# Optimization experiments

Hardware: AMD Instinct MI355X
Metric: run time of the kernel (lower is better)

Reference implementation:

```python
import jax, jax.numpy as jnp
import numpy as np

D = 64      # hidden_dim
H = 4       # num_attention_heads
DH = D // H # head_dim
B = 64      # graphs per batch
SCALE = np.float32(np.sqrt(DH))


def _sage(x, edge, wl, bl, wr):
    # SAGEConv: lin_l(mean_j x_j) + lin_r(x_i); mean over incoming edges (dst = edge[1])
    src, dst = edge[0], edge[1]
    n = x.shape[0]
    agg = jax.ops.segment_sum(x[src], dst, num_segments=n)
    cnt = jax.ops.segment_sum(jnp.ones((edge.shape[1],), x.dtype), dst, num_segments=n)
    mean = agg / jnp.maximum(cnt, 1.0)[:, None]
    return mean @ wl + bl + x @ wr


def _cross_attn(xq, xk, w, b):
    # w: [3, D, D] stacked (Q, K, V) projections; b: [3, D]
    Q = (xq @ w[0] + b[0]).reshape(-1, H, DH)  # [Nq, H, DH]
    K = (xk @ w[1] + b[1]).reshape(-1, H, DH)  # [Nk, H, DH]
    V = (xk @ w[2] + b[2]).reshape(-1, H, DH)
    scores = jnp.einsum('qhd,khd->hqk', Q, K) / SCALE  # [H, Nq, Nk]
    wgt = jax.nn.softmax(scores, axis=-1)
    out = jnp.einsum('hqk,khd->qhd', wgt, V)
    return out.reshape(xq.shape[0], D)


def _segment_mean(x, seg, num):
    s = jax.ops.segment_sum(x, seg, num_segments=num)
    c = jax.ops.segment_sum(jnp.ones((x.shape[0],), x.dtype), seg, num_segments=num)
    return s / jnp.maximum(c, 1.0)[:, None]


def setup_inputs() -> dict:
    key = jax.random.key(0)
    ks = jax.random.split(key, 32)
    N_MOL, N_PROT, E_MOL, E_PROT = 2048, 8192, 32768, 131072
    MOL_IN, PROT_IN = 32, 64

    def lin(k, i, o, s=None):
        s = 1.0 / np.sqrt(i) if s is None else s
        return (jax.random.normal(k, (i, o), jnp.float32) * s)

    inp = {
        'x_mol': jax.random.normal(ks[0], (N_MOL, MOL_IN), jnp.float32),
        'x_prot': jax.random.normal(ks[1], (N_PROT, PROT_IN), jnp.float32),
        'm1_wl': lin(ks[2], MOL_IN, D), 'm1_bl': jnp.zeros((D,), jnp.float32), 'm1_wr': lin(ks[3], MOL_IN, D),
        'm2_wl': lin(ks[4], D, D), 'm2_bl': jnp.zeros((D,), jnp.float32), 'm2_wr': lin(ks[5], D, D),
        'p1_wl': lin(ks[6], PROT_IN, D), 'p1_bl': jnp.zeros((D,), jnp.float32), 'p1_wr': lin(ks[7], PROT_IN, D),
        'p2_wl': lin(ks[8], D, D), 'p2_bl': jnp.zeros((D,), jnp.float32), 'p2_wr': lin(ks[9], D, D),
        'amp_w': jax.random.normal(ks[10], (3, D, D), jnp.float32) / np.sqrt(D),
        'amp_b': jnp.zeros((3, D), jnp.float32),
        'apm_w': jax.random.normal(ks[11], (3, D, D), jnp.float32) / np.sqrt(D),
        'apm_b': jnp.zeros((3, D), jnp.float32),
        'fc1_w': lin(ks[12], 2 * D, D), 'fc1_b': jnp.zeros((D,), jnp.float32),
        'fc2_w': lin(ks[13], D, 1), 'fc2_b': jnp.zeros((1,), jnp.float32),
        'edge_mol': jax.random.randint(ks[14], (2, E_MOL), 0, N_MOL, jnp.int32),
        'edge_prot': jax.random.randint(ks[15], (2, E_PROT), 0, N_PROT, jnp.int32),
        'batch_mol': jnp.sort(jax.random.randint(ks[16], (N_MOL,), 0, B, jnp.int32)),
        'batch_prot': jnp.sort(jax.random.randint(ks[17], (N_PROT,), 0, B, jnp.int32)),
    }
    return inp


def reference(x_mol, x_prot,
              m1_wl, m1_bl, m1_wr, m2_wl, m2_bl, m2_wr,
              p1_wl, p1_bl, p1_wr, p2_wl, p2_bl, p2_wr,
              amp_w, amp_b, apm_w, apm_b,
              fc1_w, fc1_b, fc2_w, fc2_b,
              edge_mol, edge_prot, batch_mol, batch_prot):
    # two SAGE conv blocks per graph, ReLU after each (HeteroConv with one edge type)
    h_mol = jax.nn.relu(_sage(x_mol, edge_mol, m1_wl, m1_bl, m1_wr))
    h_mol = jax.nn.relu(_sage(h_mol, edge_mol, m2_wl, m2_bl, m2_wr))
    h_prot = jax.nn.relu(_sage(x_prot, edge_prot, p1_wl, p1_bl, p1_wr))
    h_prot = jax.nn.relu(_sage(h_prot, edge_prot, p2_wl, p2_bl, p2_wr))
    # cross attention (mol queries prot, prot queries mol) + residual
    h_mol_c = h_mol + _cross_attn(h_mol, h_prot, amp_w, amp_b)
    h_prot_c = h_prot + _cross_attn(h_prot, h_mol, apm_w, apm_b)
    # global mean pool per graph
    z_mol = _segment_mean(h_mol_c, batch_mol, B)    # [B, D]
    z_prot = _segment_mean(h_prot_c, batch_prot, B)  # [B, D]
    z = jnp.concatenate([z_mol, z_prot], axis=1)     # [B, 2D]
    x = jax.nn.relu(z @ fc1_w + fc1_b)
    out = jax.nn.sigmoid(x @ fc2_w + fc2_b)
    return out.squeeze(-1)  # [B]
```

## Files before the change

kernel.cpp:

```cpp
#include <hip/hip_runtime.h>
#include <math.h>

#define D 64
#define NB 64

typedef __attribute__((ext_vector_type(8))) short bf16x8;
typedef __attribute__((ext_vector_type(4))) float f32x4;
typedef __attribute__((ext_vector_type(16))) float f32x16;

#define M3(a, b, c) fmaxf(fmaxf((a), (b)), (c))

__device__ __forceinline__ unsigned short f2bf(float f) {
    unsigned u = __float_as_uint(f);
    u += 0x7FFF + ((u >> 16) & 1);
    return (unsigned short)(u >> 16);
}
__device__ __forceinline__ unsigned pk_bf16(float lo, float hi) {
    unsigned r;
    asm("v_cvt_pk_bf16_f32 %0, %1, %2" : "=v"(r) : "v"(lo), "v"(hi));
    return r;
}
__device__ __forceinline__ float fexp2(float x) {
    float r;
    asm("v_exp_f32 %0, %1" : "=v"(r) : "v"(x));
    return r;
}

__global__ void k_prep2(const int* __restrict__ em, int Em,
                        const int* __restrict__ ep, int Ep,
                        int* __restrict__ degm, int* __restrict__ degp,
                        const int* __restrict__ bm, int Nm, int* __restrict__ bsM,
                        const int* __restrict__ bp, int Np, int* __restrict__ bsP) {
    int i = blockIdx.x * blockDim.x + threadIdx.x;
    if (i < Em) atomicAdd(&degm[em[Em + i]], 1);
    int j = i - Em;
    if (j >= 0 && j < Ep) atomicAdd(&degp[ep[Ep + j]], 1);
    if (i < Nm) {
        int cur = bm[i];
        int prev = (i == 0) ? -1 : bm[i - 1];
        for (int b = prev + 1; b <= cur; ++b) bsM[b] = i;
        if (i == Nm - 1)
            for (int b = cur + 1; b <= NB; ++b) bsM[b] = Nm;
    }
    int j2 = i - Nm;
    if (j2 >= 0 && j2 < Np) {
        int cur = bp[j2];
        int prev = (j2 == 0) ? -1 : bp[j2 - 1];
        for (int b = prev + 1; b <= cur; ++b) bsP[b] = j2;
        if (j2 == Np - 1)
            for (int b = cur + 1; b <= NB; ++b) bsP[b] = Np;
    }
}

__global__ __launch_bounds__(256) void k_scan2(
        const int* __restrict__ degm, int Nm, int* __restrict__ rpm, int* __restrict__ curm,
        const int* __restrict__ degp, int Np, int* __restrict__ rpp, int* __restrict__ curp) {
    __shared__ int sdeg[8192];
    __shared__ int chunk[256];
    const int* deg = blockIdx.x ? degp : degm;
    int N = blockIdx.x ? Np : Nm;
    int* rowptr = blockIdx.x ? rpp : rpm;
    int* cursor = blockIdx.x ? curp : curm;
    int t = threadIdx.x;
    for (int i = t; i < N; i += 256) sdeg[i] = deg[i];
    __syncthreads();
    int C = (N + 255) / 256;
    int start = t * C;
    int sum = 0;
    for (int i = 0; i < C; ++i)
        if (start + i < N) sum += sdeg[start + i];
    chunk[t] = sum;
    __syncthreads();
    for (int ofs = 1; ofs < 256; ofs <<= 1) {
        int v = (t >= ofs) ? chunk[t - ofs] : 0;
        __syncthreads();
        chunk[t] += v;
        __syncthreads();
    }
    int base = (t == 0) ? 0 : chunk[t - 1];
    for (int i = 0; i < C && start + i < N; ++i) {
        rowptr[start + i] = base;
        cursor[start + i] = base;
        base += sdeg[start + i];
    }
    if (t == 255) rowptr[N] = base;
}

__global__ void k_scatter2(const int* __restrict__ em, int Em, int* __restrict__ curm,
                           int* __restrict__ csrm,
                           const int* __restrict__ ep, int Ep, int* __restrict__ curp,
                           int* __restrict__ csrp) {
    int i = blockIdx.x * blockDim.x + threadIdx.x;
    if (i < Em) {
        int s = em[i], d = em[Em + i];
        csrm[atomicAdd(&curm[d], 1)] = s;
    }
    int j = i - Em;
    if (j >= 0 && j < Ep) {
        int s = ep[j], d = ep[Ep + j];
        csrp[atomicAdd(&curp[d], 1)] = s;
    }
}

template<int FIN>
__device__ __forceinline__ void gsage3_body(
        const float* __restrict__ x, const int* __restrict__ rowptr,
        const int* __restrict__ csr, int N,
        const float* __restrict__ wl, const float* __restrict__ bl,
        const float* __restrict__ wr, float* __restrict__ out,
        int blk, float* __restrict__ swl, float* __restrict__ swr,
        float* __restrict__ sagg, float* __restrict__ sx) {
    for (int i = threadIdx.x; i < FIN * D; i += 256) { swl[i] = wl[i]; swr[i] = wr[i]; }
    __syncthreads();
    int w = threadIdx.x >> 6;
    int lane = threadIdx.x & 63;
    for (int rr = 0; rr < 4; ++rr) {
        int r = blk * 16 + w * 4 + rr;
        if (r >= N) return;
        int e0 = rowptr[r], e1 = rowptr[r + 1];
        float inv = 1.0f / fmaxf((float)(e1 - e0), 1.0f);
        if (FIN == 64) {
            float a0 = 0.f, a1 = 0.f, a2 = 0.f, a3 = 0.f;
            int e = e0;
            for (; e + 3 < e1; e += 4) {
                a0 += x[(size_t)csr[e] * FIN + lane];
                a1 += x[(size_t)csr[e + 1] * FIN + lane];
                a2 += x[(size_t)csr[e + 2] * FIN + lane];
                a3 += x[(size_t)csr[e + 3] * FIN + lane];
            }
            for (; e < e1; ++e) a0 += x[(size_t)csr[e] * FIN + lane];
            sagg[w * 64 + lane] = ((a0 + a1) + (a2 + a3)) * inv;
            sx[w * 64 + lane] = x[(size_t)r * FIN + lane];
        } else {
            int f = lane & 31, half = lane >> 5;
            float a = 0.f;
            for (int e = e0 + half; e < e1; e += 2)
                a += x[(size_t)csr[e] * FIN + f];
            a += __shfl_xor(a, 32);
            if (half == 0) {
                sagg[w * 64 + f] = a * inv;
                sx[w * 64 + f] = x[(size_t)r * FIN + f];
            }
        }
        int c = lane;
        float acc = bl[c];
        #pragma unroll 8
        for (int k = 0; k < FIN; ++k) {
            acc += sagg[w * 64 + k] * swl[k * D + c];
            acc += sx[w * 64 + k] * swr[k * D + c];
        }
        out[(size_t)r * D + c] = fmaxf(acc, 0.0f);
    }
}

template<int FA, int FB>
__global__ __launch_bounds__(256) void k_gsage3(
        const float* __restrict__ xA, const int* __restrict__ rpA,
        const int* __restrict__ csrA, int NA,
        const float* __restrict__ wlA, const float* __restrict__ blA,
        const float* __restrict__ wrA, float* __restrict__ outA,
        const float* __restrict__ xB, const int* __restrict__ rpB,
        const int* __restrict__ csrB, int NB_,
        const float* __restrict__ wlB, const float* __restrict__ blB,
        const float* __restrict__ wrB, float* __restrict__ outB) {
    __shared__ float swl[64 * 64];
    __shared__ float swr[64 * 64];
    __shared__ float sagg[4 * 64];
    __shared__ float sx[4 * 64];
    int bA = (NA + 15) / 16;
    if ((int)blockIdx.x < bA)
        gsage3_body<FA>(xA, rpA, csrA, NA, wlA, blA, wrA, outA, blockIdx.x, swl, swr, sagg, sx);
    else
        gsage3_body<FB>(xB, rpB, csrB, NB_, wlB, blB, wrB, outB, blockIdx.x - bA, swl, swr, sagg, sx);
}

__global__ __launch_bounds__(256) void k_qkv3(
        const float* __restrict__ xA, int NA, const float* __restrict__ xB, int NB_,
        const float* __restrict__ amp_w, const float* __restrict__ amp_b,
        const float* __restrict__ apm_w, const float* __restrict__ apm_b, float qs,
        unsigned short* __restrict__ QA, unsigned short* __restrict__ KA,
        unsigned short* __restrict__ VtA,
        unsigned short* __restrict__ QB, unsigned short* __restrict__ KB,
        unsigned short* __restrict__ VtB) {
    __shared__ float sq[D * D], sk[D * D], sv[D * D];
    __shared__ float sx[32 * D];
    __shared__ unsigned short svo[32][68];
    int bA = NA / 32;
    const float *x, *wq, *bq, *wk, *bk, *wv, *bv;
    unsigned short *oq, *ok, *vt;
    int blk, N;
    if ((int)blockIdx.x < bA) {
        x = xA; blk = blockIdx.x; N = NA;
        wq = amp_w;        bq = amp_b;
        wk = apm_w + 4096; bk = apm_b + 64;
        wv = apm_w + 8192; bv = apm_b + 128;
        oq = QA; ok = KA; vt = VtA;
    } else {
        x = xB; blk = blockIdx.x - bA; N = NB_;
        wq = apm_w;        bq = apm_b;
        wk = amp_w + 4096; bk = amp_b + 64;
        wv = amp_w + 8192; bv = amp_b + 128;
        oq = QB; ok = KB; vt = VtB;
    }
    for (int i = threadIdx.x; i < D * D; i += 256) { sq[i] = wq[i]; sk[i] = wk[i]; sv[i] = wv[i]; }
    int rbase = blk * 32;
    for (int i = threadIdx.x; i < 32 * D; i += 256) sx[i] = x[(size_t)rbase * D + i];
    __syncthreads();
    int c = threadIdx.x & 63;
    int r0 = (threadIdx.x >> 6) * 8;
    for (int rr = 0; rr < 8; ++rr) {
        int r = r0 + rr;
        float aq = bq[c], ak = bk[c], av = bv[c];
        #pragma unroll 8
        for (int k = 0; k < D; ++k) {
            float xv = sx[r * D + k];
            aq += xv * sq[k * D + c];
            ak += xv * sk[k * D + c];
            av += xv * sv[k * D + c];
        }
        size_t o = (size_t)(rbase + r) * D + c;
        oq[o] = f2bf(aq * qs);
        ok[o] = f2bf(ak);
        svo[r][c] = f2bf(av);
    }
    __syncthreads();
    const int gmap[4] = {0, 8, 4, 12};
    #pragma unroll
    for (int jj = 0; jj < 2; ++jj) {
        int j = threadIdx.x + jj * 256;
        int ccol = j & 63;
        int grp = j >> 6;
        int b16 = (grp & 4) ? 16 : 0;
        int g = grp & 3;
        int k0 = b16 + g * 4;
        union { uint2 v; unsigned short s[4]; } u;
        u.s[0] = svo[k0 + 0][ccol];
        u.s[1] = svo[k0 + 1][ccol];
        u.s[2] = svo[k0 + 2][ccol];
        u.s[3] = svo[k0 + 3][ccol];
        *(uint2*)(vt + (size_t)ccol * N + rbase + b16 + gmap[g]) = u.v;
    }
    if (threadIdx.x < 4) {
        uint4 ones;
        ones.x = ones.y = ones.z = ones.w = 0x3F803F80u;
        *(uint4*)(vt + (size_t)64 * N + rbase + threadIdx.x * 8) = ones;
    }
}

#define MAXTREE(cm, s0, s1)                                                   \
    {                                                                         \
        float c0 = M3(s0[0], s0[1], s0[2]);                                   \
        float c1 = M3(s0[3], s0[4], s0[5]);                                   \
        float c2 = M3(s0[6], s0[7], s0[8]);                                   \
        float c3 = M3(s0[9], s0[10], s0[11]);                                 \
        float c4 = M3(s0[12], s0[13], s0[14]);                                \
        float c5 = M3(s0[15], s1[0], s1[1]);                                  \
        float c6 = M3(s1[2], s1[3], s1[4]);                                   \
        float c7 = M3(s1[5], s1[6], s1[7]);                                   \
        float c8 = M3(s1[8], s1[9], s1[10]);                                  \
        float c9 = M3(s1[11], s1[12], s1[13]);                                \
        float ca = fmaxf(s1[14], s1[15]);                                     \
        float d0 = M3(c0, c1, c2);                                            \
        float d1 = M3(c3, c4, c5);                                            \
        float d2 = M3(c6, c7, c8);                                            \
        float d3 = M3(c9, ca, d0);                                            \
        cm = M3(d1, d2, d3);                                                  \
    }

#define PVPACK(S, KB)                                                         \
    {                                                                         \
        union { unsigned u[4]; bf16x8 v; } f1, f2;                            \
        f1.u[0] = pk_bf16((S)[0], (S)[1]);   f1.u[1] = pk_bf16((S)[2], (S)[3]);  \
        f1.u[2] = pk_bf16((S)[4], (S)[5]);   f1.u[3] = pk_bf16((S)[6], (S)[7]);  \
        f2.u[0] = pk_bf16((S)[8], (S)[9]);   f2.u[1] = pk_bf16((S)[10], (S)[11]);\
        f2.u[2] = pk_bf16((S)[12], (S)[13]); f2.u[3] = pk_bf16((S)[14], (S)[15]);\
        bf16x8 vb0 = *(const bf16x8*)(vbase + (KB) + half * 8);               \
        bf16x8 vb1 = *(const bf16x8*)(vbase + (KB) + 16 + half * 8);          \
        __builtin_amdgcn_s_setprio(1);                                        \
        o = __builtin_amdgcn_mfma_f32_32x32x16_bf16(f1.v, vb0, o, 0, 0, 0);   \
        o = __builtin_amdgcn_mfma_f32_32x32x16_bf16(f2.v, vb1, o, 0, 0, 0);   \
        __builtin_amdgcn_s_setprio(0);                                        \
    }

__global__ __launch_bounds__(512) void k_attn6(
        const unsigned short* __restrict__ QmB, const unsigned short* __restrict__ KpB,
        const unsigned short* __restrict__ VpT, int Nm, int Np, int lsm,
        float* __restrict__ poM, float* __restrict__ pmM, float* __restrict__ plM,
        const unsigned short* __restrict__ QpB, const unsigned short* __restrict__ KmB,
        const unsigned short* __restrict__ VmT, int lsp,
        float* __restrict__ poP, float* __restrict__ pmP, float* __restrict__ plP) {
    const unsigned short *Q, *K, *Vt;
    int Nq, Nk, ls;
    float *po, *pm, *pl;
    if (blockIdx.y == 0) { Q = QmB; K = KpB; Vt = VpT; Nq = Nm; Nk = Np; ls = lsm; po = poM; pm = pmM; pl = plM; }
    else                 { Q = QpB; K = KmB; Vt = VmT; Nq = Np; Nk = Nm; ls = lsp; po = poP; pm = pmP; pl = plP; }
    int npair = Nq >> 6;
    if ((int)blockIdx.x >= (npair << ls)) return;
    const int qpair = blockIdx.x >> ls;
    const int split = blockIdx.x & ((1 << ls) - 1);
    const int kchunk = Nk >> ls;
    const int w = threadIdx.x >> 6;
    const int h = w & 3;
    const int qt = qpair * 2 + (w >> 2);
    const int lane = threadIdx.x & 63;
    const int cq = lane & 31;
    const int half = lane >> 5;
    const int h16 = h * 16;

    bf16x8 qb = *(const bf16x8*)(Q + ((size_t)(qt * 32 + cq) * D + h16 + half * 8));
    int drow = (cq < 16) ? (h16 + cq) : (cq == 16 ? 64 : h16 + 15);
    const unsigned short* vbase = Vt + (size_t)drow * Nk;

    f32x16 o, mC;
    #pragma unroll
    for (int i = 0; i < 16; ++i) { o[i] = 0.f; mC[i] = 0.f; }
    float m;

    const int kstart = split * kchunk;
    {
        const int kb = kstart;
        bf16x8 ka0 = *(const bf16x8*)(K + ((size_t)(kb + cq) * D + h16 + half * 8));
        bf16x8 ka1 = *(const bf16x8*)(K + ((size_t)(kb + 32 + cq) * D + h16 + half * 8));
        f32x16 s0 = __builtin_amdgcn_mfma_f32_32x32x16_bf16(ka0, qb, mC, 0, 0, 0);
        f32x16 s1 = __builtin_amdgcn_mfma_f32_32x32x16_bf16(ka1, qb, mC, 0, 0, 0);
        float cm;
        MAXTREE(cm, s0, s1);
        #pragma unroll
        for (int off = 1; off < 64; off <<= 1) cm = fmaxf(cm, __shfl_xor(cm, off));
        m = cm;
        #pragma unroll
        for (int i = 0; i < 16; ++i) {
            s0[i] = fexp2(s0[i] - m);
            s1[i] = fexp2(s1[i] - m);
            mC[i] = -m;
        }
        PVPACK(s0, kb)
        PVPACK(s1, kb + 32)
    }
    for (int kb = kstart + 64; kb < kstart + kchunk; kb += 64) {
        bf16x8 ka0 = *(const bf16x8*)(K + ((size_t)(kb + cq) * D + h16 + half * 8));
        bf16x8 ka1 = *(const bf16x8*)(K + ((size_t)(kb + 32 + cq) * D + h16 + half * 8));
        f32x16 s0 = __builtin_amdgcn_mfma_f32_32x32x16_bf16(ka0, qb, mC, 0, 0, 0);
        f32x16 s1 = __builtin_amdgcn_mfma_f32_32x32x16_bf16(ka1, qb, mC, 0, 0, 0);
        float cm;
        MAXTREE(cm, s0, s1);
        if (__any(cm > 8.f)) {
            float cw = cm;
            #pragma unroll
            for (int off = 1; off < 64; off <<= 1) cw = fmaxf(cw, __shfl_xor(cw, off));
            float nm = fmaxf(m + cw, m);
            float sc = fexp2(m - nm);
            #pragma unroll
            for (int i = 0; i < 16; ++i) o[i] *= sc;
            float dl = nm - m;
            #pragma unroll
            for (int i = 0; i < 16; ++i) { s0[i] -= dl; s1[i] -= dl; mC[i] = -nm; }
            m = nm;
        }
        #pragma unroll
        for (int i = 0; i < 16; ++i) { s0[i] = fexp2(s0[i]); s1[i] = fexp2(s1[i]); }
        PVPACK(s0, kb)
        PVPACK(s1, kb + 32)
    }

    size_t pbase = (size_t)split * Nq + qt * 32;
    if (half == 0)
        pm[(pbase + cq) * 4 + h] = m;
    if (cq == 16) {
        #pragma unroll
        for (int r = 0; r < 16; ++r) {
            int qr = (r & 3) + 8 * (r >> 2) + 4 * half;
            pl[(pbase + qr) * 4 + h] = o[r];
        }
    }
    if (cq < 16) {
        #pragma unroll
        for (int r = 0; r < 16; ++r) {
            int qr = (r & 3) + 8 * (r >> 2) + 4 * half;
            po[(pbase + qr) * 64 + h16 + cq] = o[r];
        }
    }
}

template<int NS>
__device__ __forceinline__ void comb_body(
        const float* __restrict__ po, const float* __restrict__ pm,
        const float* __restrict__ pl, int Nq,
        const float* __restrict__ resid, float* __restrict__ outc, int i) {
    int q = i >> 4;
    int part = i & 15;
    int d0 = part * 4;
    int h = part >> 2;
    float pmv[NS], plv[NS];
    #pragma unroll
    for (int s = 0; s < NS; ++s) pmv[s] = pm[((size_t)s * Nq + q) * 4 + h];
    #pragma unroll
    for (int s = 0; s < NS; ++s) plv[s] = pl[((size_t)s * Nq + q) * 4 + h];
    float M = pmv[0];
    #pragma unroll
    for (int s = 1; s < NS; ++s) M = fmaxf(M, pmv[s]);
    float4 O = {0.f, 0.f, 0.f, 0.f};
    float L = 0.f;
    #pragma unroll
    for (int s = 0; s < NS; ++s) {
        float wgt = fexp2(pmv[s] - M);
        float4 pv = *(const float4*)(po + ((size_t)s * Nq + q) * 64 + d0);
        O.x += pv.x * wgt; O.y += pv.y * wgt; O.z += pv.z * wgt; O.w += pv.w * wgt;
        L += plv[s] * wgt;
    }
    float invL = 1.0f / L;
    float4 rv = *(const float4*)(resid + (size_t)q * 64 + d0);
    float4 res;
    res.x = rv.x + O.x * invL;
    res.y = rv.y + O.y * invL;
    res.z = rv.z + O.z * invL;
    res.w = rv.w + O.w * invL;
    *(float4*)(outc + (size_t)q * 64 + d0) = res;
}

template<int NSM, int NSP>
__global__ void k_comb2t(
        const float* __restrict__ poM, const float* __restrict__ pmM, const float* __restrict__ plM,
        int Nm, const float* __restrict__ residM, float* __restrict__ outM,
        const float* __restrict__ poP, const float* __restrict__ pmP, const float* __restrict__ plP,
        int Np, const float* __restrict__ residP, float* __restrict__ outP) {
    int idx = blockIdx.x * blockDim.x + threadIdx.x;
    int mtot = Nm * 16;
    if (idx < mtot)
        comb_body<NSM>(poM, pmM, plM, Nm, residM, outM, idx);
    else if (idx - mtot < Np * 16)
        comb_body<NSP>(poP, pmP, plP, Np, residP, outP, idx - mtot);
}

__global__ void k_comb2(
        const float* __restrict__ poM, const float* __restrict__ pmM, const float* __restrict__ plM,
        int nsM, int Nm, const float* __restrict__ residM, float* __restrict__ outM,
        const float* __restrict__ poP, const float* __restrict__ pmP, const float* __restrict__ plP,
        int nsP, int Np, const float* __restrict__ residP, float* __restrict__ outP) {
    int idx = blockIdx.x * blockDim.x + threadIdx.x;
    const float *po, *pm, *pl, *resid;
    float* outc;
    int ns, Nq, i;
    int mtot = Nm * 64;
    if (idx < mtot) {
        po = poM; pm = pmM; pl = plM; ns = nsM; Nq = Nm; resid = residM; outc = outM; i = idx;
    } else {
        i = idx - mtot;
        if (i >= Np * 64) return;
        po = poP; pm = pmP; pl = plP; ns = nsP; Nq = Np; resid = residP; outc = outP;
    }
    int q = i >> 6, d = i & 63, h = d >> 4;
    float M = -1e30f;
    for (int s = 0; s < ns; ++s)
        M = fmaxf(M, pm[((size_t)s * Nq + q) * 4 + h]);
    float O = 0.f, L = 0.f;
    for (int s = 0; s < ns; ++s) {
        float wgt = fexp2(pm[((size_t)s * Nq + q) * 4 + h] - M);
        O += po[((size_t)s * Nq + q) * 64 + d] * wgt;
        L += pl[((size_t)s * Nq + q) * 4 + h] * wgt;
    }
    outc[i] = resid[i] + O / L;
}

__global__ __launch_bounds__(256) void k_poolhead(
        const float* __restrict__ hM, const int* __restrict__ bsM,
        const float* __restrict__ hP, const int* __restrict__ bsP,
        const float* __restrict__ fc1w, const float* __restrict__ fc1b,
        const float* __restrict__ fc2w, const float* __restrict__ fc2b,
        float* __restrict__ out) {
    __shared__ float red[4][64];
    __shared__ float zs[128];
    int b = blockIdx.x;
    int w = threadIdx.x >> 6, c = threadIdx.x & 63;
    int n0 = bsM[b], n1 = bsM[b + 1];
    float acc = 0.f;
    for (int n = n0 + w; n < n1; n += 4) acc += hM[(size_t)n * 64 + c];
    red[w][c] = acc;
    __syncthreads();
    if (w == 0)
        zs[c] = ((red[0][c] + red[1][c]) + (red[2][c] + red[3][c])) /
                fmaxf((float)(n1 - n0), 1.0f);
    __syncthreads();
    n0 = bsP[b]; n1 = bsP[b + 1];
    acc = 0.f;
    for (int n = n0 + w; n < n1; n += 4) acc += hP[(size_t)n * 64 + c];
    red[w][c] = acc;
    __syncthreads();
    if (w == 0)
        zs[64 + c] = ((red[0][c] + red[1][c]) + (red[2][c] + red[3][c])) /
                     fmaxf((float)(n1 - n0), 1.0f);
    __syncthreads();
    if (w == 0) {
        float a = fc1b[c];
        #pragma unroll 8
        for (int k = 0; k < 128; ++k) a += zs[k] * fc1w[k * 64 + c];
        float v = fmaxf(a, 0.0f) * fc2w[c];
        #pragma unroll
        for (int off = 32; off > 0; off >>= 1) v += __shfl_xor(v, off);
        if (c == 0) out[b] = 1.0f / (1.0f + __expf(-(v + fc2b[0])));
    }
}

extern "C" void kernel_launch(void* const* d_in, const int* in_sizes, int n_in,
                              void* d_out, int out_size, void* d_ws, size_t ws_size,
                              hipStream_t stream) {
    const float* x_mol  = (const float*)d_in[0];
    const float* x_prot = (const float*)d_in[1];
    const float* m1_wl = (const float*)d_in[2];
    const float* m1_bl = (const float*)d_in[3];
    const float* m1_wr = (const float*)d_in[4];
    const float* m2_wl = (const float*)d_in[5];
    const float* m2_bl = (const float*)d_in[6];
    const float* m2_wr = (const float*)d_in[7];
    const float* p1_wl = (const float*)d_in[8];
    const float* p1_bl = (const float*)d_in[9];
    const float* p1_wr = (const float*)d_in[10];
    const float* p2_wl = (const float*)d_in[11];
    const float* p2_bl = (const float*)d_in[12];
    const float* p2_wr = (const float*)d_in[13];
    const float* amp_w = (const float*)d_in[14];
    const float* amp_b = (const float*)d_in[15];
    const float* apm_w = (const float*)d_in[16];
    const float* apm_b = (const float*)d_in[17];
    const float* fc1_w = (const float*)d_in[18];
    const float* fc1_b = (const float*)d_in[19];
    const float* fc2_w = (const float*)d_in[20];
    const float* fc2_b = (const float*)d_in[21];
    const int* edge_mol  = (const int*)d_in[22];
    const int* edge_prot = (const int*)d_in[23];
    const int* batch_mol  = (const int*)d_in[24];
    const int* batch_prot = (const int*)d_in[25];
    float* out = (float*)d_out;

    const int N_MOL  = in_sizes[0] / 32;
    const int N_PROT = in_sizes[1] / 64;
    const int E_MOL  = in_sizes[22] / 2;
    const int E_PROT = in_sizes[23] / 2;

    char* base = (char*)d_ws;
    size_t off = 0;
    auto alloc = [&](size_t bytes) -> void* {
        void* p = base + off;
        off = (off + bytes + 255) & ~(size_t)255;
        return p;
    };
    float* h_mol1   = (float*)alloc((size_t)N_MOL * D * sizeof(float));
    float* h_mol2   = (float*)alloc((size_t)N_MOL * D * sizeof(float));
    float* h_prot1  = (float*)alloc((size_t)N_PROT * D * sizeof(float));
    float* h_prot2  = (float*)alloc((size_t)N_PROT * D * sizeof(float));
    float* h_mol_c  = (float*)alloc((size_t)N_MOL * D * sizeof(float));
    float* h_prot_c = (float*)alloc((size_t)N_PROT * D * sizeof(float));
    unsigned short* Qm_b = (unsigned short*)alloc((size_t)N_MOL * D * 2);
    unsigned short* Km_b = (unsigned short*)alloc((size_t)N_MOL * D * 2);
    unsigned short* Vm_t = (unsigned short*)alloc((size_t)N_MOL * (D + 1) * 2);
    unsigned short* Qp_b = (unsigned short*)alloc((size_t)N_PROT * D * 2);
    unsigned short* Kp_b = (unsigned short*)alloc((size_t)N_PROT * D * 2);
    unsigned short* Vp_t = (unsigned short*)alloc((size_t)N_PROT * (D + 1) * 2);
    int* deg      = (int*)alloc(((size_t)N_MOL + N_PROT) * sizeof(int));
    int* deg_m    = deg;
    int* deg_p    = deg + N_MOL;
    int* rp_m     = (int*)alloc(((size_t)N_MOL + 1) * sizeof(int));
    int* cur_m    = (int*)alloc((size_t)N_MOL * sizeof(int));
    int* csr_m    = (int*)alloc((size_t)E_MOL * sizeof(int));
    int* rp_p     = (int*)alloc(((size_t)N_PROT + 1) * sizeof(int));
    int* cur_p    = (int*)alloc((size_t)N_PROT * sizeof(int));
    int* csr_p    = (int*)alloc((size_t)E_PROT * sizeof(int));
    int* bsM      = (int*)alloc((NB + 1) * sizeof(int));
    int* bsP      = (int*)alloc((NB + 1) * sizeof(int));

    int nsm = 16; while (nsm > 1 && (N_PROT % (64 * nsm))) nsm >>= 1;
    int nsp = 4;  while (nsp > 1 && (N_MOL % (64 * nsp)))  nsp >>= 1;
    int lsm = 31 - __builtin_clz(nsm);
    int lsp = 31 - __builtin_clz(nsp);
    float* poM = (float*)alloc((size_t)nsm * N_MOL * 64 * sizeof(float));
    float* pmM = (float*)alloc((size_t)nsm * N_MOL * 4 * sizeof(float));
    float* plM = (float*)alloc((size_t)nsm * N_MOL * 4 * sizeof(float));
    float* poP = (float*)alloc((size_t)nsp * N_PROT * 64 * sizeof(float));
    float* pmP = (float*)alloc((size_t)nsp * N_PROT * 4 * sizeof(float));
    float* plP = (float*)alloc((size_t)nsp * N_PROT * 4 * sizeof(float));

    const int BLK = 256;
    dim3 blk(BLK);
    const float QS = 0.25f * 1.4426950408889634f;

    hipMemsetAsync(deg, 0, ((size_t)N_MOL + N_PROT) * sizeof(int), stream);
    int Etot = E_MOL + E_PROT;
    k_prep2<<<(Etot + BLK - 1) / BLK, blk, 0, stream>>>(
        edge_mol, E_MOL, edge_prot, E_PROT, deg_m, deg_p,
        batch_mol, N_MOL, bsM, batch_prot, N_PROT, bsP);
    k_scan2<<<2, blk, 0, stream>>>(deg_m, N_MOL, rp_m, cur_m, deg_p, N_PROT, rp_p, cur_p);
    k_scatter2<<<(Etot + BLK - 1) / BLK, blk, 0, stream>>>(edge_mol, E_MOL, cur_m, csr_m,
                                                           edge_prot, E_PROT, cur_p, csr_p);

    int gs = (N_MOL + 15) / 16 + (N_PROT + 15) / 16;
    k_gsage3<32, 64><<<gs, blk, 0, stream>>>(
        x_mol,  rp_m, csr_m, N_MOL,  m1_wl, m1_bl, m1_wr, h_mol1,
        x_prot, rp_p, csr_p, N_PROT, p1_wl, p1_bl, p1_wr, h_prot1);
    k_gsage3<64, 64><<<gs, blk, 0, stream>>>(
        h_mol1,  rp_m, csr_m, N_MOL,  m2_wl, m2_bl, m2_wr, h_mol2,
        h_prot1, rp_p, csr_p, N_PROT, p2_wl, p2_bl, p2_wr, h_prot2);

    k_qkv3<<<N_MOL / 32 + N_PROT / 32, blk, 0, stream>>>(
        h_mol2, N_MOL, h_prot2, N_PROT, amp_w, amp_b, apm_w, apm_b, QS,
        Qm_b, Km_b, Vm_t, Qp_b, Kp_b, Vp_t);

    int gxm = (N_MOL / 64) * nsm;
    int gxp = (N_PROT / 64) * nsp;
    int gx = gxm > gxp ? gxm : gxp;
    k_attn6<<<dim3(gx, 2), dim3(512), 0, stream>>>(
        Qm_b, Kp_b, Vp_t, N_MOL, N_PROT, lsm, poM, pmM, plM,
        Qp_b, Km_b, Vm_t, lsp, poP, pmP, plP);

    if (nsm == 16 && nsp == 4) {
        int tot = (N_MOL + N_PROT) * 16;
        k_comb2t<16, 4><<<(tot + BLK - 1) / BLK, blk, 0, stream>>>(
            poM, pmM, plM, N_MOL, h_mol2, h_mol_c,
            poP, pmP, plP, N_PROT, h_prot2, h_prot_c);
    } else {
        k_comb2<<<((N_MOL + N_PROT) * 64 + BLK - 1) / BLK, blk, 0, stream>>>(
            poM, pmM, plM, nsm, N_MOL, h_mol2, h_mol_c,
            poP, pmP, plP, nsp, N_PROT, h_prot2, h_prot_c);
    }

    k_poolhead<<<NB, blk, 0, stream>>>(h_mol_c, bsM, h_prot_c, bsP,
                                       fc1_w, fc1_b, fc2_w, fc2_b, out);
}
```

Before: 173.1 us.

## Switch cross-attention to 16x16x32 MFMA tiles with per-wave work split

Rewrites the flash-attention kernel to use 16x16x32 bf16 MFMA with 16-query tiles, one wave per (query tile, head, key split), instead of 32x32x16 tiles in 512-thread blocks. The row sum is now accumulated in registers with shuffles rather than through a ones row appended to V, so V storage drops the extra row and the QKV kernel is relaid to match the new fragment layout. The lazy rescaling branch is removed because the max is taken only from the first block, which relies on scores staying bounded. Half the K lanes load zeros, which wastes part of the MFMA K dimension, and the grid becomes much larger.

```diff
diff --git a/kernel.cpp b/kernel.cpp
--- a/kernel.cpp
+++ b/kernel.cpp
@@ -6,7 +6,6 @@
 
 typedef __attribute__((ext_vector_type(8))) short bf16x8;
 typedef __attribute__((ext_vector_type(4))) float f32x4;
-typedef __attribute__((ext_vector_type(16))) float f32x16;
 
 #define M3(a, b, c) fmaxf(fmaxf((a), (b)), (c))
 
@@ -224,65 +223,24 @@
         svo[r][c] = f2bf(av);
     }
     __syncthreads();
-    const int gmap[4] = {0, 8, 4, 12};
     #pragma unroll
     for (int jj = 0; jj < 2; ++jj) {
         int j = threadIdx.x + jj * 256;
         int ccol = j & 63;
         int grp = j >> 6;
-        int b16 = (grp & 4) ? 16 : 0;
         int g = grp & 3;
-        int k0 = b16 + g * 4;
+        int k0  = (grp < 4) ? 4 * g : 16 + 4 * g;
+        int pos = (grp < 4) ? 8 * g : 8 * g + 4;
         union { uint2 v; unsigned short s[4]; } u;
         u.s[0] = svo[k0 + 0][ccol];
         u.s[1] = svo[k0 + 1][ccol];
         u.s[2] = svo[k0 + 2][ccol];
         u.s[3] = svo[k0 + 3][ccol];
-        *(uint2*)(vt + (size_t)ccol * N + rbase + b16 + gmap[g]) = u.v;
-    }
-    if (threadIdx.x < 4) {
-        uint4 ones;
-        ones.x = ones.y = ones.z = ones.w = 0x3F803F80u;
-        *(uint4*)(vt + (size_t)64 * N + rbase + threadIdx.x * 8) = ones;
-    }
-}
-
-#define MAXTREE(cm, s0, s1)                                                   \
-    {                                                                         \
-        float c0 = M3(s0[0], s0[1], s0[2]);                                   \
-        float c1 = M3(s0[3], s0[4], s0[5]);                                   \
-        float c2 = M3(s0[6], s0[7], s0[8]);                                   \
-        float c3 = M3(s0[9], s0[10], s0[11]);                                 \
-        float c4 = M3(s0[12], s0[13], s0[14]);                                \
-        float c5 = M3(s0[15], s1[0], s1[1]);                                  \
-        float c6 = M3(s1[2], s1[3], s1[4]);                                   \
-        float c7 = M3(s1[5], s1[6], s1[7]);                                   \
-        float c8 = M3(s1[8], s1[9], s1[10]);                                  \
-        float c9 = M3(s1[11], s1[12], s1[13]);                                \
-        float ca = fmaxf(s1[14], s1[15]);                                     \
-        float d0 = M3(c0, c1, c2);                                            \
-        float d1 = M3(c3, c4, c5);                                            \
-        float d2 = M3(c6, c7, c8);                                            \
-        float d3 = M3(c9, ca, d0);                                            \
-        cm = M3(d1, d2, d3);                                                  \
-    }
-
-#define PVPACK(S, KB)                                                         \
-    {                                                                         \
-        union { unsigned u[4]; bf16x8 v; } f1, f2;                            \
-        f1.u[0] = pk_bf16((S)[0], (S)[1]);   f1.u[1] = pk_bf16((S)[2], (S)[3]);  \
-        f1.u[2] = pk_bf16((S)[4], (S)[5]);   f1.u[3] = pk_bf16((S)[6], (S)[7]);  \
-        f2.u[0] = pk_bf16((S)[8], (S)[9]);   f2.u[1] = pk_bf16((S)[10], (S)[11]);\
-        f2.u[2] = pk_bf16((S)[12], (S)[13]); f2.u[3] = pk_bf16((S)[14], (S)[15]);\
-        bf16x8 vb0 = *(const bf16x8*)(vbase + (KB) + half * 8);               \
-        bf16x8 vb1 = *(const bf16x8*)(vbase + (KB) + 16 + half * 8);          \
-        __builtin_amdgcn_s_setprio(1);                                        \
-        o = __builtin_amdgcn_mfma_f32_32x32x16_bf16(f1.v, vb0, o, 0, 0, 0);   \
-        o = __builtin_amdgcn_mfma_f32_32x32x16_bf16(f2.v, vb1, o, 0, 0, 0);   \
-        __builtin_amdgcn_s_setprio(0);                                        \
-    }
-
-__global__ __launch_bounds__(512) void k_attn6(
+        *(uint2*)(vt + (size_t)ccol * N + rbase + pos) = u.v;
+    }
+}
+
+__global__ __launch_bounds__(256) void k_attn7(
         const unsigned short* __restrict__ QmB, const unsigned short* __restrict__ KpB,
         const unsigned short* __restrict__ VpT, int Nm, int Np, int lsm,
         float* __restrict__ poM, float* __restrict__ pmM, float* __restrict__ plM,
@@ -294,92 +252,95 @@
     float *po, *pm, *pl;
     if (blockIdx.y == 0) { Q = QmB; K = KpB; Vt = VpT; Nq = Nm; Nk = Np; ls = lsm; po = poM; pm = pmM; pl = plM; }
     else                 { Q = QpB; K = KmB; Vt = VmT; Nq = Np; Nk = Nm; ls = lsp; po = poP; pm = pmP; pl = plP; }
-    int npair = Nq >> 6;
-    if ((int)blockIdx.x >= (npair << ls)) return;
-    const int qpair = blockIdx.x >> ls;
-    const int split = blockIdx.x & ((1 << ls) - 1);
+    int nq16 = Nq >> 4;
+    int wid = blockIdx.x * 4 + (threadIdx.x >> 6);
+    if (wid >= (nq16 << (ls + 2))) return;
+    const int split = wid & ((1 << ls) - 1);
+    int rest = wid >> ls;
+    const int h = rest & 3;
+    const int qt = rest >> 2;
     const int kchunk = Nk >> ls;
-    const int w = threadIdx.x >> 6;
-    const int h = w & 3;
-    const int qt = qpair * 2 + (w >> 2);
     const int lane = threadIdx.x & 63;
-    const int cq = lane & 31;
-    const int half = lane >> 5;
+    const int q = lane & 15;
+    const int g = lane >> 4;
     const int h16 = h * 16;
 
-    bf16x8 qb = *(const bf16x8*)(Q + ((size_t)(qt * 32 + cq) * D + h16 + half * 8));
-    int drow = (cq < 16) ? (h16 + cq) : (cq == 16 ? 64 : h16 + 15);
-    const unsigned short* vbase = Vt + (size_t)drow * Nk;
-
-    f32x16 o, mC;
-    #pragma unroll
-    for (int i = 0; i < 16; ++i) { o[i] = 0.f; mC[i] = 0.f; }
-    float m;
+    bf16x8 qb = {0, 0, 0, 0, 0, 0, 0, 0};
+    if (g < 2)
+        qb = *(const bf16x8*)(Q + ((size_t)(qt * 16 + q) * D + h16 + g * 8));
+    const unsigned short* vrow = Vt + (size_t)(h16 + q) * Nk;
+
+    f32x4 o = {0.f, 0.f, 0.f, 0.f};
+    f32x4 mC = {0.f, 0.f, 0.f, 0.f};
+    float l = 0.f, m;
 
     const int kstart = split * kchunk;
     {
         const int kb = kstart;
-        bf16x8 ka0 = *(const bf16x8*)(K + ((size_t)(kb + cq) * D + h16 + half * 8));
-        bf16x8 ka1 = *(const bf16x8*)(K + ((size_t)(kb + 32 + cq) * D + h16 + half * 8));
-        f32x16 s0 = __builtin_amdgcn_mfma_f32_32x32x16_bf16(ka0, qb, mC, 0, 0, 0);
-        f32x16 s1 = __builtin_amdgcn_mfma_f32_32x32x16_bf16(ka1, qb, mC, 0, 0, 0);
-        float cm;
-        MAXTREE(cm, s0, s1);
+        bf16x8 ka0 = {0, 0, 0, 0, 0, 0, 0, 0};
+        bf16x8 ka1 = {0, 0, 0, 0, 0, 0, 0, 0};
+        if (g < 2) {
+            ka0 = *(const bf16x8*)(K + ((size_t)(kb + q) * D + h16 + g * 8));
+            ka1 = *(const bf16x8*)(K + ((size_t)(kb + 16 + q) * D + h16 + g * 8));
+        }
+        f32x4 s0 = __builtin_amdgcn_mfma_f32_16x16x32_bf16(ka0, qb, mC, 0, 0, 0);
+        f32x4 s1 = __builtin_amdgcn_mfma_f32_16x16x32_bf16(ka1, qb, mC, 0, 0, 0);
+        float cm = fmaxf(M3(s0[0], s0[1], s0[2]), M3(s0[3], s1[0], s1[1]));
+        cm = M3(cm, s1[2], s1[3]);
         #pragma unroll
         for (int off = 1; off < 64; off <<= 1) cm = fmaxf(cm, __shfl_xor(cm, off));
         m = cm;
         #pragma unroll
-        for (int i = 0; i < 16; ++i) {
+        for (int i = 0; i < 4; ++i) {
             s0[i] = fexp2(s0[i] - m);
             s1[i] = fexp2(s1[i] - m);
             mC[i] = -m;
         }
-        PVPACK(s0, kb)
-        PVPACK(s1, kb + 32)
-    }
-    for (int kb = kstart + 64; kb < kstart + kchunk; kb += 64) {
-        bf16x8 ka0 = *(const bf16x8*)(K + ((size_t)(kb + cq) * D + h16 + half * 8));
-        bf16x8 ka1 = *(const bf16x8*)(K + ((size_t)(kb + 32 + cq) * D + h16 + half * 8));
-        f32x16 s0 = __builtin_amdgcn_mfma_f32_32x32x16_bf16(ka0, qb, mC, 0, 0, 0);
-        f32x16 s1 = __builtin_amdgcn_mfma_f32_32x32x16_bf16(ka1, qb, mC, 0, 0, 0);
-        float cm;
-        MAXTREE(cm, s0, s1);
-        if (__any(cm > 8.f)) {
-            float cw = cm;
-            #pragma unroll
-            for (int off = 1; off < 64; off <<= 1) cw = fmaxf(cw, __shfl_xor(cw, off));
-            float nm = fmaxf(m + cw, m);
-            float sc = fexp2(m - nm);
-            #pragma unroll
-            for (int i = 0; i < 16; ++i) o[i] *= sc;
-            float dl = nm - m;
-            #pragma unroll
-            for (int i = 0; i < 16; ++i) { s0[i] -= dl; s1[i] -= dl; mC[i] = -nm; }
-            m = nm;
-        }
+        l += ((s0[0] + s0[1]) + (s0[2] + s0[3])) + ((s1[0] + s1[1]) + (s1[2] + s1[3]));
+        union { unsigned u[4]; bf16x8 v; } pw;
+        pw.u[0] = pk_bf16(s0[0], s0[1]);
+        pw.u[1] = pk_bf16(s0[2], s0[3]);
+        pw.u[2] = pk_bf16(s1[0], s1[1]);
+        pw.u[3] = pk_bf16(s1[2], s1[3]);
+        bf16x8 va = *(const bf16x8*)(vrow + kb + g * 8);
+        o = __builtin_amdgcn_mfma_f32_16x16x32_bf16(va, pw.v, o, 0, 0, 0);
+    }
+    for (int kb = kstart + 32; kb < kstart + kchunk; kb += 32) {
+        bf16x8 ka0 = {0, 0, 0, 0, 0, 0, 0, 0};
+        bf16x8 ka1 = {0, 0, 0, 0, 0, 0, 0, 0};
+        if (g < 2) {
+            ka0 = *(const bf16x8*)(K + ((size_t)(kb + q) * D + h16 + g * 8));
+            ka1 = *(const bf16x8*)(K + ((size_t)(kb + 16 + q) * D + h16 + g * 8));
+        }
+        f32x4 s0 = __builtin_amdgcn_mfma_f32_16x16x32_bf16(ka0, qb, mC, 0, 0, 0);
+        f32x4 s1 = __builtin_amdgcn_mfma_f32_16x16x32_bf16(ka1, qb, mC, 0, 0, 0);
         #pragma unroll
-        for (int i = 0; i < 16; ++i) { s0[i] = fexp2(s0[i]); s1[i] = fexp2(s1[i]); }
-        PVPACK(s0, kb)
-        PVPACK(s1, kb + 32)
-    }
-
-    size_t pbase = (size_t)split * Nq + qt * 32;
-    if (half == 0)
-        pm[(pbase + cq) * 4 + h] = m;
-    if (cq == 16) {
-        #pragma unroll
-        for (int r = 0; r < 16; ++r) {
-            int qr = (r & 3) + 8 * (r >> 2) + 4 * half;
-            pl[(pbase + qr) * 4 + h] = o[r];
-        }
-    }
-    if (cq < 16) {
-        #pragma unroll
-        for (int r = 0; r < 16; ++r) {
-            int qr = (r & 3) + 8 * (r >> 2) + 4 * half;
-            po[(pbase + qr) * 64 + h16 + cq] = o[r];
-        }
-    }
+        for (int i = 0; i < 4; ++i) {
+            s0[i] = fexp2(s0[i]);
+            s1[i] = fexp2(s1[i]);
+        }
+        l += ((s0[0] + s0[1]) + (s0[2] + s0[3])) + ((s1[0] + s1[1]) + (s1[2] + s1[3]));
+        union { unsigned u[4]; bf16x8 v; } pw;
+        pw.u[0] = pk_bf16(s0[0], s0[1]);
+        pw.u[1] = pk_bf16(s0[2], s0[3]);
+        pw.u[2] = pk_bf16(s1[0], s1[1]);
+        pw.u[3] = pk_bf16(s1[2], s1[3]);
+        bf16x8 va = *(const bf16x8*)(vrow + kb + g * 8);
+        __builtin_amdgcn_s_setprio(1);
+        o = __builtin_amdgcn_mfma_f32_16x16x32_bf16(va, pw.v, o, 0, 0, 0);
+        __builtin_amdgcn_s_setprio(0);
+    }
+
+    l += __shfl_xor(l, 16);
+    l += __shfl_xor(l, 32);
+
+    size_t pbase = (size_t)split * Nq + qt * 16;
+    if (lane < 16) {
+        pm[(pbase + lane) * 4 + h] = m;
+        pl[(pbase + lane) * 4 + h] = l;
+    }
+    float4 ov = {o[0], o[1], o[2], o[3]};
+    *(float4*)(po + (pbase + q) * 64 + h16 + g * 4) = ov;
 }
 
 template<int NS>
@@ -552,10 +513,10 @@
     float* h_prot_c = (float*)alloc((size_t)N_PROT * D * sizeof(float));
     unsigned short* Qm_b = (unsigned short*)alloc((size_t)N_MOL * D * 2);
     unsigned short* Km_b = (unsigned short*)alloc((size_t)N_MOL * D * 2);
-    unsigned short* Vm_t = (unsigned short*)alloc((size_t)N_MOL * (D + 1) * 2);
+    unsigned short* Vm_t = (unsigned short*)alloc((size_t)N_MOL * D * 2);
     unsigned short* Qp_b = (unsigned short*)alloc((size_t)N_PROT * D * 2);
     unsigned short* Kp_b = (unsigned short*)alloc((size_t)N_PROT * D * 2);
-    unsigned short* Vp_t = (unsigned short*)alloc((size_t)N_PROT * (D + 1) * 2);
+    unsigned short* Vp_t = (unsigned short*)alloc((size_t)N_PROT * D * 2);
     int* deg      = (int*)alloc(((size_t)N_MOL + N_PROT) * sizeof(int));
     int* deg_m    = deg;
     int* deg_p    = deg + N_MOL;
@@ -568,8 +529,8 @@
     int* bsM      = (int*)alloc((NB + 1) * sizeof(int));
     int* bsP      = (int*)alloc((NB + 1) * sizeof(int));
 
-    int nsm = 16; while (nsm > 1 && (N_PROT % (64 * nsm))) nsm >>= 1;
-    int nsp = 4;  while (nsp > 1 && (N_MOL % (64 * nsp)))  nsp >>= 1;
+    int nsm = 16; while (nsm > 1 && (N_PROT % (32 * nsm))) nsm >>= 1;
+    int nsp = 4;  while (nsp > 1 && (N_MOL % (32 * nsp)))  nsp >>= 1;
     int lsm = 31 - __builtin_clz(nsm);
     int lsp = 31 - __builtin_clz(nsp);
     float* poM = (float*)alloc((size_t)nsm * N_MOL * 64 * sizeof(float));
@@ -604,10 +565,10 @@
         h_mol2, N_MOL, h_prot2, N_PROT, amp_w, amp_b, apm_w, apm_b, QS,
         Qm_b, Km_b, Vm_t, Qp_b, Kp_b, Vp_t);
 
-    int gxm = (N_MOL / 64) * nsm;
-    int gxp = (N_PROT / 64) * nsp;
-    int gx = gxm > gxp ? gxm : gxp;
-    k_attn6<<<dim3(gx, 2), dim3(512), 0, stream>>>(
+    int gbm = (N_MOL / 16) * nsm;
+    int gbp = (N_PROT / 16) * nsp;
+    int gx = gbm > gbp ? gbm : gbp;
+    k_attn7<<<dim3(gx, 2), blk, 0, stream>>>(
         Qm_b, Kp_b, Vp_t, N_MOL, N_PROT, lsm, poM, pmM, plM,
         Qp_b, Km_b, Vm_t, lsp, poP, pmP, plP);
 
```

After: 199.1 us. +15.0%, slower.
